# Performance work log

Hardware: AMD Instinct MI355X
Metric: run time of the kernel (lower is better)

Reference implementation:

```python
import jax, jax.numpy as jnp
import numpy as np

N_NODES = 20000
D = 256            # input_dim (forced by 32x16 reshape: 2*D == 512)
N_EDGES = 320000


def _init(key, shape, scale=0.02):
    return scale * jax.random.normal(key, shape, jnp.float32)


def setup_inputs() -> dict:
    key = jax.random.key(0)
    ks = jax.random.split(key, 20)
    x = jax.random.normal(ks[0], (N_NODES, D), jnp.float32)
    edge = jax.random.randint(ks[1], (N_EDGES, 2), 0, N_NODES, dtype=jnp.int64)
    params = dict(
        W_gcn=_init(ks[2], (D, 2 * D)), b_gcn=jnp.zeros((2 * D,), jnp.float32),
        conv1_w=_init(ks[3], (1, 1, 3, 3)), conv1_b=jnp.zeros((1,), jnp.float32),
        conv2_w=_init(ks[4], (1, 1, 3, 3)), conv2_b=jnp.zeros((1,), jnp.float32),
        Wc1=_init(ks[5], (2 * D, 2 * D)), bc1=jnp.zeros((2 * D,), jnp.float32),
        Wc2=_init(ks[6], (2 * D, 2 * D)), bc2=jnp.zeros((2 * D,), jnp.float32),
        Wc3=_init(ks[7], (2 * D, 2 * D)), bc3=jnp.zeros((2 * D,), jnp.float32),
        Wp1=_init(ks[8], (4 * D, 2 * D)), bp1=jnp.zeros((2 * D,), jnp.float32),
        Wp2=_init(ks[9], (2 * D, D)), bp2=jnp.zeros((D,), jnp.float32),
        Wp3=_init(ks[10], (D, D // 2)), bp3=jnp.zeros((D // 2,), jnp.float32),
        Wp4=_init(ks[11], (D // 2, 2)), bp4=jnp.zeros((2,), jnp.float32),
    )
    return dict(x=x, edge=edge, **params)


def _gcn_conv(x, edge, W, b):
    # PyG GCNConv: add self-loops, symmetric deg^-1/2 normalization, scatter-add at dst
    src, dst = edge[:, 0], edge[:, 1]
    loops = jnp.arange(N_NODES, dtype=edge.dtype)
    src = jnp.concatenate([src, loops])
    dst = jnp.concatenate([dst, loops])
    xw = x @ W                                              # [N, 2D]
    deg = jax.ops.segment_sum(jnp.ones_like(dst, jnp.float32), dst, N_NODES)
    dinv = jnp.where(deg > 0, jax.lax.rsqrt(jnp.maximum(deg, 1e-12)), 0.0)
    norm = dinv[src] * dinv[dst]                            # [E+N]
    agg = jax.ops.segment_sum(norm[:, None] * xw[src], dst, N_NODES)
    return agg + b


def reference(x, edge, W_gcn, b_gcn, conv1_w, conv1_b, conv2_w, conv2_b,
              Wc1, bc1, Wc2, bc2, Wc3, bc3,
              Wp1, bp1, Wp2, bp2, Wp3, bp3, Wp4, bp4):
    # First stage: GCNConv + ReLU, then sum readout over nodes -> [1, 2D]
    h = jax.nn.relu(_gcn_conv(x, edge, W_gcn, b_gcn))
    h = jnp.sum(h, axis=0, keepdims=True)                   # [1, 512]

    img = h.reshape(1, 1, 32, 16)
    dn = ('NCHW', 'OIHW', 'NCHW')
    c = jax.nn.relu(jax.lax.conv_general_dilated(img, conv1_w, (1, 1), 'SAME', dimension_numbers=dn) + conv1_b.reshape(1, -1, 1, 1))
    c = jax.nn.relu(jax.lax.conv_general_dilated(c, conv2_w, (1, 1), 'SAME', dimension_numbers=dn) + conv2_b.reshape(1, -1, 1, 1))
    high_conf = jax.nn.softmax(c.reshape(1, -1), axis=1)    # [1, 512]

    # Second stage, branch B: 3-layer MLP with softmax
    f = jax.nn.relu(h @ Wc1 + bc1)
    f = jax.nn.relu(f @ Wc2 + bc2)
    front = jax.nn.softmax(f @ Wc3 + bc3, axis=1)           # [1, 512]

    complete = jnp.concatenate([high_conf, front], axis=1)  # [1, 1024]

    # Predictor MLP: 1024 -> 512 -> 256 -> 128 -> 2, sigmoid
    p = jax.nn.relu(complete @ Wp1 + bp1)
    p = jax.nn.relu(p @ Wp2 + bp2)
    p = jax.nn.relu(p @ Wp3 + bp3)
    pre = jax.nn.sigmoid(p @ Wp4 + bp4)                     # [1, 2]
    return pre
```

## Files before the change

### kernel.cpp

```cpp
#include <hip/hip_runtime.h>

#define N_NODES 20000
#define N_EDGES 320000
#define DD      256
#define D2      512
#define BCAP    64

typedef short short8 __attribute__((ext_vector_type(8)));
typedef float f32x4  __attribute__((ext_vector_type(4)));
typedef float f32x2  __attribute__((ext_vector_type(2)));

__device__ __forceinline__ unsigned f2b(float f) {
    unsigned u = __float_as_uint(f);
    u = u + 0x7fffu + ((u >> 16) & 1u);
    return u >> 16;
}

__device__ __forceinline__ unsigned decode_cnt(unsigned c) {
    return (c >= 0xAAAAAAAAu) ? c - 0xAAAAAAAAu : c;
}

__device__ __forceinline__ void packW(const float* __restrict__ src, unsigned* __restrict__ dst,
                                      int i, int logn) {
    int N = 1 << logn;
    int c = i & (N - 1);
    int kp = i >> logn;
    const float* r0 = src + ((size_t)kp << (logn + 1)) + c;
    float4 a = *(const float4*)r0;
    float4 b = *(const float4*)(r0 + N);
    uint4 o;
    o.x = f2b(a.x) | (f2b(b.x) << 16);
    o.y = f2b(a.y) | (f2b(b.y) << 16);
    o.z = f2b(a.z) | (f2b(b.z) << 16);
    o.w = f2b(a.w) | (f2b(b.w) << 16);
    *(uint4*)(dst + i) = o;
}

__global__ void k1_prep(const int* __restrict__ edge, unsigned* __restrict__ cnt,
                        int* __restrict__ csr, const float* __restrict__ x,
                        const float* __restrict__ Wg, unsigned short* __restrict__ WT,
                        unsigned* __restrict__ xf8, int* __restrict__ zbase,
                        const float* __restrict__ Wc1, const float* __restrict__ Wc2,
                        const float* __restrict__ Wc3, const float* __restrict__ Wp1,
                        const float* __restrict__ Wp2, const float* __restrict__ Wp3,
                        unsigned* __restrict__ Wc1p, unsigned* __restrict__ Wc2p,
                        unsigned* __restrict__ Wc3p, unsigned* __restrict__ Wp1p,
                        unsigned* __restrict__ Wp2p, unsigned* __restrict__ Wp3p) {
    int blk = blockIdx.x, tid = threadIdx.x;
    if (blk < 1250) {
        int e = blk * 256 + tid;
        if (e < N_EDGES) {
            int s = edge[2 * e], d = edge[2 * e + 1];
            unsigned pos = atomicAdd(&cnt[d], 1u);
            unsigned rel = decode_cnt(pos);
            if (rel < BCAP) csr[d * BCAP + rel] = s;
        }
    } else if (blk < 1282) {
        int i = (blk - 1250) * 256 + tid;
        #pragma unroll
        for (int r = 0; r < 16; r++) {
            int idx = i + r * 8192;
            int k = idx >> 9, n = idx & 511;
            WT[n * 256 + k] = (unsigned short)f2b(Wg[idx]);
        }
    } else if (blk < 6282) {
        int i = (blk - 1282) * 256 + tid;
        float4 v = ((const float4*)x)[i];
        unsigned o = 0;
        o = __builtin_amdgcn_cvt_pk_fp8_f32(v.x, v.y, o, false);
        o = __builtin_amdgcn_cvt_pk_fp8_f32(v.z, v.w, o, true);
        xf8[i] = o;
    } else if (blk < 6285) {
        int i = (blk - 6282) * 256 + tid;
        if (i < 640) zbase[i] = 0;
    } else if (blk < 6413) { packW(Wc1, Wc1p, ((blk - 6285) * 256 + tid) * 4, 9); }
    else if (blk < 6541) { packW(Wc2, Wc2p, ((blk - 6413) * 256 + tid) * 4, 9); }
    else if (blk < 6669) { packW(Wc3, Wc3p, ((blk - 6541) * 256 + tid) * 4, 9); }
    else if (blk < 6925) { packW(Wp1, Wp1p, ((blk - 6669) * 256 + tid) * 4, 9); }
    else if (blk < 6989) { packW(Wp2, Wp2p, ((blk - 6925) * 256 + tid) * 4, 8); }
    else                 { packW(Wp3, Wp3p, ((blk - 6989) * 256 + tid) * 4, 7); }
}

__device__ __forceinline__ float dinv_of(const unsigned* cnt, int n) {
    return rsqrtf((float)(decode_cnt(cnt[n]) + 1u));
}
__device__ __forceinline__ void acc16p(f32x2* a, float w, uint4 u) {
    f32x2 wv = {w, w};
    unsigned uu[4] = {u.x, u.y, u.z, u.w};
    #pragma unroll
    for (int q = 0; q < 4; q++) {
        a[q * 2 + 0] += wv * __builtin_amdgcn_cvt_pk_f32_fp8(uu[q], false);
        a[q * 2 + 1] += wv * __builtin_amdgcn_cvt_pk_f32_fp8(uu[q], true);
    }
}

__global__ void k4_agg(const unsigned* __restrict__ cnt, const int* __restrict__ csr,
                       const unsigned char* __restrict__ xf8,
                       unsigned short* __restrict__ aggX) {
    int wid = threadIdx.x >> 6, lane = threadIdx.x & 63;
    int g = lane >> 4, l16 = lane & 15;
    int n = blockIdx.x * 4 + wid;
    f32x2 a[8];
    #pragma unroll
    for (int j = 0; j < 8; j++) a[j] = (f32x2){0.f, 0.f};
    if (n < N_NODES) {
        int deg = (int)decode_cnt(cnt[n]);
        if (deg > BCAP) deg = BCAP;
        const int* bkt = csr + n * BCAP;
        int e = 0;
        for (; e + 8 <= deg; e += 8) {
            int s0 = bkt[e + g], s1 = bkt[e + 4 + g];
            uint4 u0 = *(const uint4*)(xf8 + (size_t)s0 * DD + l16 * 16);
            uint4 u1 = *(const uint4*)(xf8 + (size_t)s1 * DD + l16 * 16);
            float w0 = dinv_of(cnt, s0), w1 = dinv_of(cnt, s1);
            acc16p(a, w0, u0); acc16p(a, w1, u1);
        }
        for (; e < deg; e += 4) {
            int idx = e + g;
            int cidx = idx < deg ? idx : deg - 1;
            int s = bkt[cidx];
            uint4 u = *(const uint4*)(xf8 + (size_t)s * DD + l16 * 16);
            float w = idx < deg ? dinv_of(cnt, s) : 0.f;
            acc16p(a, w, u);
        }
        #pragma unroll
        for (int j = 0; j < 8; j++) {
            a[j].x += __shfl_xor(a[j].x, 16, 64);
            a[j].x += __shfl_xor(a[j].x, 32, 64);
            a[j].y += __shfl_xor(a[j].y, 16, 64);
            a[j].y += __shfl_xor(a[j].y, 32, 64);
        }
        float dn = dinv_of(cnt, n), dn2 = dn * dn;
        f32x2 dv = {dn, dn}, dv2 = {dn2, dn2};
        uint4 u = *(const uint4*)(xf8 + (size_t)n * DD + l16 * 16);
        unsigned uu[4] = {u.x, u.y, u.z, u.w};
        #pragma unroll
        for (int q = 0; q < 4; q++) {
            a[q * 2 + 0] = dv * a[q * 2 + 0] + dv2 * __builtin_amdgcn_cvt_pk_f32_fp8(uu[q], false);
            a[q * 2 + 1] = dv * a[q * 2 + 1] + dv2 * __builtin_amdgcn_cvt_pk_f32_fp8(uu[q], true);
        }
    }
    if (g == 0) {
        unsigned o[8];
        #pragma unroll
        for (int j = 0; j < 8; j++) o[j] = f2b(a[j].x) | (f2b(a[j].y) << 16);
        uint4* dst = (uint4*)(aggX + (size_t)n * DD + l16 * 16);
        dst[0] = make_uint4(o[0], o[1], o[2], o[3]);
        dst[1] = make_uint4(o[4], o[5], o[6], o[7]);
    }
}

#define TN 128
#define BPAD 268
__global__ void __launch_bounds__(256, 2)
k5_gemm(const unsigned short* __restrict__ aggX, const unsigned short* __restrict__ WT,
        const float* __restrict__ bg, float* __restrict__ h) {
    __shared__ unsigned short bsh[TN * BPAD];
    __shared__ float hblk[TN];
    int tid = threadIdx.x;
    int rowblk = blockIdx.x;
    int ct = blockIdx.y;
    #pragma unroll
    for (int i = 0; i < 16; i++) {
        int c = tid + i * 256;
        int r = c >> 5;
        int kc = (c & 31) << 3;
        *(short8*)(&bsh[r * BPAD + kc]) = *(const short8*)(WT + (size_t)(ct * TN + r) * DD + kc);
    }
    if (tid < TN) hblk[tid] = 0.f;
    __syncthreads();

    int w = tid >> 6, lane = tid & 63;
    int quad = lane >> 4, l15 = lane & 15;
    int row0 = rowblk * 128 + w * 32 + l15;
    f32x4 acc[2][8];
    #pragma unroll
    for (int s = 0; s < 2; s++)
        #pragma unroll
        for (int nt = 0; nt < 8; nt++) acc[s][nt] = (f32x4){0.f, 0.f, 0.f, 0.f};
    #pragma unroll
    for (int kt = 0; kt < 8; kt++) {
        short8 a0 = *(const short8*)(aggX + (size_t)row0 * DD + kt * 32 + quad * 8);
        short8 a1 = *(const short8*)(aggX + (size_t)(row0 + 16) * DD + kt * 32 + quad * 8);
        #pragma unroll
        for (int nt = 0; nt < 8; nt++) {
            short8 b = *(const short8*)(&bsh[(nt * 16 + l15) * BPAD + kt * 32 + quad * 8]);
            acc[0][nt] = __builtin_amdgcn_mfma_f32_16x16x32_bf16(a0, b, acc[0][nt], 0, 0, 0);
            acc[1][nt] = __builtin_amdgcn_mfma_f32_16x16x32_bf16(a1, b, acc[1][nt], 0, 0, 0);
        }
    }
    #pragma unroll
    for (int s = 0; s < 2; s++) {
        int rowbase = rowblk * 128 + w * 32 + s * 16 + quad * 4;
        #pragma unroll
        for (int nt = 0; nt < 8; nt++) {
            int cl = nt * 16 + l15;
            float bias = bg[ct * TN + cl];
            float sum = 0.f;
            #pragma unroll
            for (int r = 0; r < 4; r++) {
                if (rowbase + r < N_NODES) {
                    float v = acc[s][nt][r] + bias;
                    sum += v > 0.f ? v : 0.f;
                }
            }
            sum += __shfl_xor(sum, 16, 64);
            sum += __shfl_xor(sum, 32, 64);
            if (quad == 0) atomicAdd(&hblk[cl], sum);
        }
    }
    __syncthreads();
    if (tid < TN) atomicAdd(&h[ct * TN + tid], hblk[tid]);
}

#define TB 16u
__device__ __forceinline__ void gbar(unsigned* bar, int idx) {
    __syncthreads();
    if (threadIdx.x == 0) {
        __threadfence();
        __hip_atomic_fetch_add(&bar[idx * 16], 1u, __ATOMIC_RELEASE, __HIP_MEMORY_SCOPE_AGENT);
        while (__hip_atomic_load(&bar[idx * 16], __ATOMIC_ACQUIRE, __HIP_MEMORY_SCOPE_AGENT) < TB)
            __builtin_amdgcn_s_sleep(2);
    }
    __syncthreads();
}

__device__ __forceinline__ float conv3(const float* im, const float* wgt, int idx) {
    int y = idx >> 4, x = idx & 15;
    float s = 0.f;
    #pragma unroll
    for (int dy = -1; dy <= 1; dy++)
        #pragma unroll
        for (int dx = -1; dx <= 1; dx++) {
            int yy = y + dy, xx = x + dx;
            if (yy >= 0 && yy < 32 && xx >= 0 && xx < 16)
                s += wgt[(dy + 1) * 3 + (dx + 1)] * im[yy * 16 + xx];
        }
    return s;
}

__device__ __forceinline__ void mv32(const float* vin, const unsigned* __restrict__ Wp,
                                     int Kh, int N, int cb, float* part, float* outv) {
    int t = threadIdx.x;
    int c = cb + (t & 31), sl = t >> 5;
    int kpn = Kh >> 3;
    const unsigned* wp = Wp + (size_t)(sl * kpn) * N + c;
    float acc = 0.f;
    #pragma unroll 8
    for (int j = 0; j < kpn; j++) {
        unsigned u = wp[(size_t)j * N];
        int k = (sl * kpn + j) * 2;
        acc += vin[k] * __uint_as_float(u << 16) + vin[k + 1] * __uint_as_float(u & 0xffff0000u);
    }
    part[t] = acc;
    __syncthreads();
    if (t < 32) {
        float s = part[t];
        #pragma unroll
        for (int q = 1; q < 8; q++) s += part[t + q * 32];
        outv[cb + t] = s;
    }
}

__global__ void __launch_bounds__(256)
kt_tail(const float* __restrict__ h,
        const float* __restrict__ c1w, const float* __restrict__ c1b,
        const float* __restrict__ c2w, const float* __restrict__ c2b,
        const float* __restrict__ bc1, const float* __restrict__ bc2, const float* __restrict__ bc3,
        const unsigned* __restrict__ Wc1p, const unsigned* __restrict__ Wc2p,
        const unsigned* __restrict__ Wc3p, const unsigned* __restrict__ Wp1p,
        const unsigned* __restrict__ Wp2p, const unsigned* __restrict__ Wp3p,
        const float* __restrict__ bp1, const float* __restrict__ bp2, const float* __restrict__ bp3,
        const float* __restrict__ Wp4, const float* __restrict__ bp4,
        float* __restrict__ f1raw, float* __restrict__ f2raw, float* __restrict__ l3raw,
        float* __restrict__ p1raw, float* __restrict__ p2raw,
        float* __restrict__ out, unsigned* __restrict__ bar) {
    __shared__ float himg[512], vin[512], part[256], compL[1024], red[256];
    int b = blockIdx.x, t = threadIdx.x;
    himg[t] = h[t]; himg[t + 256] = h[t + 256];
    __syncthreads();

    mv32(himg, Wc1p, 256, 512, b * 32, part, f1raw);
    gbar(bar, 0);

    vin[t] = fmaxf(f1raw[t] + bc1[t], 0.f);
    vin[t + 256] = fmaxf(f1raw[t + 256] + bc1[t + 256], 0.f);
    __syncthreads();
    mv32(vin, Wc2p, 256, 512, b * 32, part, f2raw);
    gbar(bar, 1);

    vin[t] = fmaxf(f2raw[t] + bc2[t], 0.f);
    vin[t + 256] = fmaxf(f2raw[t + 256] + bc2[t + 256], 0.f);
    __syncthreads();
    mv32(vin, Wc3p, 256, 512, b * 32, part, l3raw);
    gbar(bar, 2);

    {
        float cb1 = c1b[0], cb2 = c2b[0];
        vin[t] = fmaxf(conv3(himg, c1w, t) + cb1, 0.f);
        vin[t + 256] = fmaxf(conv3(himg, c1w, t + 256) + cb1, 0.f);
        __syncthreads();
        float v0 = fmaxf(conv3(vin, c2w, t) + cb2, 0.f);
        float v1 = fmaxf(conv3(vin, c2w, t + 256) + cb2, 0.f);
        red[t] = fmaxf(v0, v1); __syncthreads();
        for (int off = 128; off > 0; off >>= 1) { if (t < off) red[t] = fmaxf(red[t], red[t + off]); __syncthreads(); }
        float m = red[0]; __syncthreads();
        float e0 = expf(v0 - m), e1 = expf(v1 - m);
        red[t] = e0 + e1; __syncthreads();
        for (int off = 128; off > 0; off >>= 1) { if (t < off) red[t] += red[t + off]; __syncthreads(); }
        float inv = 1.f / red[0];
        compL[t] = e0 * inv; compL[t + 256] = e1 * inv;
        __syncthreads();
        float z0 = l3raw[t] + bc3[t], z1 = l3raw[t + 256] + bc3[t + 256];
        red[t] = fmaxf(z0, z1); __syncthreads();
        for (int off = 128; off > 0; off >>= 1) { if (t < off) red[t] = fmaxf(red[t], red[t + off]); __syncthreads(); }
        float m2 = red[0]; __syncthreads();
        float e2 = expf(z0 - m2), e3 = expf(z1 - m2);
        red[t] = e2 + e3; __syncthreads();
        for (int off = 128; off > 0; off >>= 1) { if (t < off) red[t] += red[t + off]; __syncthreads(); }
        float inv2 = 1.f / red[0];
        compL[512 + t] = e2 * inv2; compL[768 + t] = e3 * inv2;
    }
    __syncthreads();

    mv32(compL, Wp1p, 512, 512, b * 32, part, p1raw);
    gbar(bar, 3);

    vin[t] = fmaxf(p1raw[t] + bp1[t], 0.f);
    vin[t + 256] = fmaxf(p1raw[t + 256] + bp1[t + 256], 0.f);
    __syncthreads();
    {
        int c = b * 16 + (t & 15), sl = t >> 4;
        const unsigned* wp = Wp2p + (size_t)(sl * 16) * 256 + c;
        float acc = 0.f;
        #pragma unroll 8
        for (int j = 0; j < 16; j++) {
            unsigned u = wp[(size_t)j * 256];
            int k = (sl * 16 + j) * 2;
            acc += vin[k] * __uint_as_float(u << 16) + vin[k + 1] * __uint_as_float(u & 0xffff0000u);
        }
        part[t] = acc;
        __syncthreads();
        if (t < 16) {
            float s = part[t];
            #pragma unroll
            for (int q = 1; q < 16; q++) s += part[t + q * 16];
            p2raw[b * 16 + t] = s;
        }
    }
    gbar(bar, 4);

    if (b == 0) {
        vin[t] = fmaxf(p2raw[t] + bp2[t], 0.f);
        __syncthreads();
        if (t < 128) {
            float acc = 0.f;
            #pragma unroll 8
            for (int kp = 0; kp < 128; kp++) {
                unsigned u = Wp3p[kp * 128 + t];
                acc += vin[2 * kp] * __uint_as_float(u << 16)
                     + vin[2 * kp + 1] * __uint_as_float(u & 0xffff0000u);
            }
            red[t] = fmaxf(acc + bp3[t], 0.f);
        }
        __syncthreads();
        if (t < 2) {
            float s = bp4[t];
            #pragma unroll 8
            for (int k = 0; k < 128; k++) s += red[k] * Wp4[k * 2 + t];
            out[t] = 1.f / (1.f + expf(-s));
        }
    }
}

extern "C" void kernel_launch(void* const* d_in, const int* in_sizes, int n_in,
                              void* d_out, int out_size, void* d_ws, size_t ws_size,
                              hipStream_t stream) {
    const float* x    = (const float*)d_in[0];
    const int*   edge = (const int*)d_in[1];
    const float* Wg   = (const float*)d_in[2];
    const float* bg   = (const float*)d_in[3];
    const float* c1w  = (const float*)d_in[4];
    const float* c1b  = (const float*)d_in[5];
    const float* c2w  = (const float*)d_in[6];
    const float* c2b  = (const float*)d_in[7];
    const float* Wc1  = (const float*)d_in[8];
    const float* bc1  = (const float*)d_in[9];
    const float* Wc2  = (const float*)d_in[10];
    const float* bc2  = (const float*)d_in[11];
    const float* Wc3  = (const float*)d_in[12];
    const float* bc3  = (const float*)d_in[13];
    const float* Wp1  = (const float*)d_in[14];
    const float* bp1  = (const float*)d_in[15];
    const float* Wp2  = (const float*)d_in[16];
    const float* bp2  = (const float*)d_in[17];
    const float* Wp3  = (const float*)d_in[18];
    const float* bp3  = (const float*)d_in[19];
    const float* Wp4  = (const float*)d_in[20];
    const float* bp4  = (const float*)d_in[21];
    float* out = (float*)d_out;

    char* ws = (char*)d_ws;
    unsigned* cnt   = (unsigned*)(ws + 0);
    float* h        = (float*)(ws + 80000);
    unsigned* bar   = (unsigned*)(ws + 82048);
    float* f1raw    = (float*)(ws + 82560);
    float* f2raw    = (float*)(ws + 84608);
    float* l3raw    = (float*)(ws + 86656);
    float* p1raw    = (float*)(ws + 88704);
    float* p2raw    = (float*)(ws + 90752);
    int*   csr      = (int*)(ws + 91904);
    unsigned short* WT   = (unsigned short*)(ws + 5211904);
    unsigned char*  xf8  = (unsigned char*)(ws + 5474048);
    unsigned short* aggX = (unsigned short*)(ws + 10594048);
    unsigned* Wc1p  = (unsigned*)(ws + 20883200);
    unsigned* Wc2p  = (unsigned*)(ws + 21407488);
    unsigned* Wc3p  = (unsigned*)(ws + 21931776);
    unsigned* Wp1p  = (unsigned*)(ws + 22456064);
    unsigned* Wp2p  = (unsigned*)(ws + 23504640);
    unsigned* Wp3p  = (unsigned*)(ws + 23766784);
    (void)ws_size; (void)in_sizes; (void)n_in; (void)out_size;

    k1_prep<<<7005, 256, 0, stream>>>(edge, cnt, csr, x, Wg, WT, (unsigned*)xf8, (int*)h,
                                      Wc1, Wc2, Wc3, Wp1, Wp2, Wp3,
                                      Wc1p, Wc2p, Wc3p, Wp1p, Wp2p, Wp3p);
    k4_agg<<<5008, 256, 0, stream>>>(cnt, csr, xf8, aggX);
    k5_gemm<<<dim3(157, 4), 256, 0, stream>>>(aggX, WT, bg, h);
    kt_tail<<<16, 256, 0, stream>>>(h, c1w, c1b, c2w, c2b, bc1, bc2, bc3,
                                    Wc1p, Wc2p, Wc3p, Wp1p, Wp2p, Wp3p,
                                    bp1, bp2, bp3, Wp4, bp4,
                                    f1raw, f2raw, l3raw, p1raw, p2raw, out, bar);
}
```

Baseline: 197.0 us.

## Fuse GEMM and MLP tail into one kernel with grid barrier; unroll aggregation by 16

Merges the GEMM-readout kernel and the tail MLP kernel into one launch. Every GEMM block bumps a completion counter, and the first 16 blocks spin on it until all 628 GEMM blocks finish, then run the tail using reused shared memory. This removes one kernel launch and its inter-kernel gap. It relies on the first 16 blocks staying resident while the others finish, which is a forward-progress assumption and a deadlock risk. The edge aggregation loop also gets an extra 16-wide unrolled stage, giving more memory loads in flight per wave.

```diff
diff --git a/kernel.cpp b/kernel.cpp
--- a/kernel.cpp
+++ b/kernel.cpp
@@ -108,6 +108,16 @@
         if (deg > BCAP) deg = BCAP;
         const int* bkt = csr + n * BCAP;
         int e = 0;
+        for (; e + 16 <= deg; e += 16) {
+            int s0 = bkt[e + g], s1 = bkt[e + 4 + g], s2 = bkt[e + 8 + g], s3 = bkt[e + 12 + g];
+            uint4 u0 = *(const uint4*)(xf8 + (size_t)s0 * DD + l16 * 16);
+            uint4 u1 = *(const uint4*)(xf8 + (size_t)s1 * DD + l16 * 16);
+            uint4 u2 = *(const uint4*)(xf8 + (size_t)s2 * DD + l16 * 16);
+            uint4 u3 = *(const uint4*)(xf8 + (size_t)s3 * DD + l16 * 16);
+            float w0 = dinv_of(cnt, s0), w1 = dinv_of(cnt, s1);
+            float w2 = dinv_of(cnt, s2), w3 = dinv_of(cnt, s3);
+            acc16p(a, w0, u0); acc16p(a, w1, u1); acc16p(a, w2, u2); acc16p(a, w3, u3);
+        }
         for (; e + 8 <= deg; e += 8) {
             int s0 = bkt[e + g], s1 = bkt[e + 4 + g];
             uint4 u0 = *(const uint4*)(xf8 + (size_t)s0 * DD + l16 * 16);
@@ -152,14 +162,79 @@
 
 #define TN 128
 #define BPAD 268
+#define TB 16u
+#define GEMM_NB 628u
+
+__device__ __forceinline__ void gbar(unsigned* bar, int idx) {
+    __syncthreads();
+    if (threadIdx.x == 0) {
+        __threadfence();
+        __hip_atomic_fetch_add(&bar[idx * 16], 1u, __ATOMIC_RELEASE, __HIP_MEMORY_SCOPE_AGENT);
+        while (__hip_atomic_load(&bar[idx * 16], __ATOMIC_ACQUIRE, __HIP_MEMORY_SCOPE_AGENT) < TB)
+            __builtin_amdgcn_s_sleep(2);
+    }
+    __syncthreads();
+}
+
+__device__ __forceinline__ float conv3(const float* im, const float* wgt, int idx) {
+    int y = idx >> 4, x = idx & 15;
+    float s = 0.f;
+    #pragma unroll
+    for (int dy = -1; dy <= 1; dy++)
+        #pragma unroll
+        for (int dx = -1; dx <= 1; dx++) {
+            int yy = y + dy, xx = x + dx;
+            if (yy >= 0 && yy < 32 && xx >= 0 && xx < 16)
+                s += wgt[(dy + 1) * 3 + (dx + 1)] * im[yy * 16 + xx];
+        }
+    return s;
+}
+
+__device__ __forceinline__ void mv32(const float* vin, const unsigned* __restrict__ Wp,
+                                     int Kh, int N, int cb, float* part, float* outv) {
+    int t = threadIdx.x;
+    int c = cb + (t & 31), sl = t >> 5;
+    int kpn = Kh >> 3;
+    const unsigned* wp = Wp + (size_t)(sl * kpn) * N + c;
+    float acc = 0.f;
+    #pragma unroll 8
+    for (int j = 0; j < kpn; j++) {
+        unsigned u = wp[(size_t)j * N];
+        int k = (sl * kpn + j) * 2;
+        acc += vin[k] * __uint_as_float(u << 16) + vin[k + 1] * __uint_as_float(u & 0xffff0000u);
+    }
+    part[t] = acc;
+    __syncthreads();
+    if (t < 32) {
+        float s = part[t];
+        #pragma unroll
+        for (int q = 1; q < 8; q++) s += part[t + q * 32];
+        outv[cb + t] = s;
+    }
+}
+
 __global__ void __launch_bounds__(256, 2)
-k5_gemm(const unsigned short* __restrict__ aggX, const unsigned short* __restrict__ WT,
-        const float* __restrict__ bg, float* __restrict__ h) {
-    __shared__ unsigned short bsh[TN * BPAD];
-    __shared__ float hblk[TN];
+k5t(const unsigned short* __restrict__ aggX, const unsigned short* __restrict__ WT,
+    const float* __restrict__ bg, float* __restrict__ h,
+    const float* __restrict__ c1w, const float* __restrict__ c1b,
+    const float* __restrict__ c2w, const float* __restrict__ c2b,
+    const float* __restrict__ bc1, const float* __restrict__ bc2, const float* __restrict__ bc3,
+    const unsigned* __restrict__ Wc1p, const unsigned* __restrict__ Wc2p,
+    const unsigned* __restrict__ Wc3p, const unsigned* __restrict__ Wp1p,
+    const unsigned* __restrict__ Wp2p, const unsigned* __restrict__ Wp3p,
+    const float* __restrict__ bp1, const float* __restrict__ bp2, const float* __restrict__ bp3,
+    const float* __restrict__ Wp4, const float* __restrict__ bp4,
+    float* __restrict__ f1raw, float* __restrict__ f2raw, float* __restrict__ l3raw,
+    float* __restrict__ p1raw, float* __restrict__ p2raw,
+    float* __restrict__ out, unsigned* __restrict__ bar) {
+    __shared__ char smem[TN * BPAD * 2 + TN * 4];
+    unsigned short* bsh = (unsigned short*)smem;
+    float* hblk = (float*)(smem + TN * BPAD * 2);
     int tid = threadIdx.x;
-    int rowblk = blockIdx.x;
-    int ct = blockIdx.y;
+    int blk = blockIdx.x;
+    int rowblk = blk % 157;
+    int ct = blk / 157;
+
     #pragma unroll
     for (int i = 0; i < 16; i++) {
         int c = tid + i * 256;
@@ -211,72 +286,25 @@
     }
     __syncthreads();
     if (tid < TN) atomicAdd(&h[ct * TN + tid], hblk[tid]);
-}
-
-#define TB 16u
-__device__ __forceinline__ void gbar(unsigned* bar, int idx) {
-    __syncthreads();
-    if (threadIdx.x == 0) {
+
+    __syncthreads();
+    if (tid == 0) {
         __threadfence();
-        __hip_atomic_fetch_add(&bar[idx * 16], 1u, __ATOMIC_RELEASE, __HIP_MEMORY_SCOPE_AGENT);
-        while (__hip_atomic_load(&bar[idx * 16], __ATOMIC_ACQUIRE, __HIP_MEMORY_SCOPE_AGENT) < TB)
+        __hip_atomic_fetch_add(&bar[5 * 16], 1u, __ATOMIC_RELEASE, __HIP_MEMORY_SCOPE_AGENT);
+    }
+    if (blk >= 16) return;
+    if (tid == 0) {
+        while (__hip_atomic_load(&bar[5 * 16], __ATOMIC_ACQUIRE, __HIP_MEMORY_SCOPE_AGENT) < GEMM_NB)
             __builtin_amdgcn_s_sleep(2);
     }
     __syncthreads();
-}
-
-__device__ __forceinline__ float conv3(const float* im, const float* wgt, int idx) {
-    int y = idx >> 4, x = idx & 15;
-    float s = 0.f;
-    #pragma unroll
-    for (int dy = -1; dy <= 1; dy++)
-        #pragma unroll
-        for (int dx = -1; dx <= 1; dx++) {
-            int yy = y + dy, xx = x + dx;
-            if (yy >= 0 && yy < 32 && xx >= 0 && xx < 16)
-                s += wgt[(dy + 1) * 3 + (dx + 1)] * im[yy * 16 + xx];
-        }
-    return s;
-}
-
-__device__ __forceinline__ void mv32(const float* vin, const unsigned* __restrict__ Wp,
-                                     int Kh, int N, int cb, float* part, float* outv) {
-    int t = threadIdx.x;
-    int c = cb + (t & 31), sl = t >> 5;
-    int kpn = Kh >> 3;
-    const unsigned* wp = Wp + (size_t)(sl * kpn) * N + c;
-    float acc = 0.f;
-    #pragma unroll 8
-    for (int j = 0; j < kpn; j++) {
-        unsigned u = wp[(size_t)j * N];
-        int k = (sl * kpn + j) * 2;
-        acc += vin[k] * __uint_as_float(u << 16) + vin[k + 1] * __uint_as_float(u & 0xffff0000u);
-    }
-    part[t] = acc;
-    __syncthreads();
-    if (t < 32) {
-        float s = part[t];
-        #pragma unroll
-        for (int q = 1; q < 8; q++) s += part[t + q * 32];
-        outv[cb + t] = s;
-    }
-}
-
-__global__ void __launch_bounds__(256)
-kt_tail(const float* __restrict__ h,
-        const float* __restrict__ c1w, const float* __restrict__ c1b,
-        const float* __restrict__ c2w, const float* __restrict__ c2b,
-        const float* __restrict__ bc1, const float* __restrict__ bc2, const float* __restrict__ bc3,
-        const unsigned* __restrict__ Wc1p, const unsigned* __restrict__ Wc2p,
-        const unsigned* __restrict__ Wc3p, const unsigned* __restrict__ Wp1p,
-        const unsigned* __restrict__ Wp2p, const unsigned* __restrict__ Wp3p,
-        const float* __restrict__ bp1, const float* __restrict__ bp2, const float* __restrict__ bp3,
-        const float* __restrict__ Wp4, const float* __restrict__ bp4,
-        float* __restrict__ f1raw, float* __restrict__ f2raw, float* __restrict__ l3raw,
-        float* __restrict__ p1raw, float* __restrict__ p2raw,
-        float* __restrict__ out, unsigned* __restrict__ bar) {
-    __shared__ float himg[512], vin[512], part[256], compL[1024], red[256];
-    int b = blockIdx.x, t = threadIdx.x;
+
+    float* himg  = (float*)smem;
+    float* vin   = (float*)(smem + 2048);
+    float* part  = (float*)(smem + 4096);
+    float* compL = (float*)(smem + 5120);
+    float* red   = (float*)(smem + 9216);
+    int b = blk, t = tid;
     himg[t] = h[t]; himg[t + 256] = h[t + 256];
     __syncthreads();
 
@@ -332,14 +360,14 @@
     {
         int c = b * 16 + (t & 15), sl = t >> 4;
         const unsigned* wp = Wp2p + (size_t)(sl * 16) * 256 + c;
-        float acc = 0.f;
+        float acc2 = 0.f;
         #pragma unroll 8
         for (int j = 0; j < 16; j++) {
             unsigned u = wp[(size_t)j * 256];
             int k = (sl * 16 + j) * 2;
-            acc += vin[k] * __uint_as_float(u << 16) + vin[k + 1] * __uint_as_float(u & 0xffff0000u);
-        }
-        part[t] = acc;
+            acc2 += vin[k] * __uint_as_float(u << 16) + vin[k + 1] * __uint_as_float(u & 0xffff0000u);
+        }
+        part[t] = acc2;
         __syncthreads();
         if (t < 16) {
             float s = part[t];
@@ -354,14 +382,14 @@
         vin[t] = fmaxf(p2raw[t] + bp2[t], 0.f);
         __syncthreads();
         if (t < 128) {
-            float acc = 0.f;
+            float acc3 = 0.f;
             #pragma unroll 8
             for (int kp = 0; kp < 128; kp++) {
                 unsigned u = Wp3p[kp * 128 + t];
-                acc += vin[2 * kp] * __uint_as_float(u << 16)
-                     + vin[2 * kp + 1] * __uint_as_float(u & 0xffff0000u);
+                acc3 += vin[2 * kp] * __uint_as_float(u << 16)
+                      + vin[2 * kp + 1] * __uint_as_float(u & 0xffff0000u);
             }
-            red[t] = fmaxf(acc + bp3[t], 0.f);
+            red[t] = fmaxf(acc3 + bp3[t], 0.f);
         }
         __syncthreads();
         if (t < 2) {
@@ -425,9 +453,9 @@
                                       Wc1, Wc2, Wc3, Wp1, Wp2, Wp3,
                                       Wc1p, Wc2p, Wc3p, Wp1p, Wp2p, Wp3p);
     k4_agg<<<5008, 256, 0, stream>>>(cnt, csr, xf8, aggX);
-    k5_gemm<<<dim3(157, 4), 256, 0, stream>>>(aggX, WT, bg, h);
-    kt_tail<<<16, 256, 0, stream>>>(h, c1w, c1b, c2w, c2b, bc1, bc2, bc3,
-                                    Wc1p, Wc2p, Wc3p, Wp1p, Wp2p, Wp3p,
-                                    bp1, bp2, bp3, Wp4, bp4,
-                                    f1raw, f2raw, l3raw, p1raw, p2raw, out, bar);
-}
+    k5t<<<628, 256, 0, stream>>>(aggX, WT, bg, h,
+                                 c1w, c1b, c2w, c2b, bc1, bc2, bc3,
+                                 Wc1p, Wc2p, Wc3p, Wp1p, Wp2p, Wp3p,
+                                 bp1, bp2, bp3, Wp4, bp4,
+                                 f1raw, f2raw, l3raw, p1raw, p2raw, out, bar);
+}
```

New measurement: 233.1 us. 18.3% more time.

## Split prep kernel into streaming and bucketing kernels; preload neighbor indices via shuffles

Applied to the files above, without the earlier changes.

The combined prep kernel is split in two. One kernel does the streaming conversions (x to fp8, weight packing, zeroing), and a separate kernel does the atomic edge bucketing, launched afterward. In the aggregation kernel, each wave loads up to 64 neighbor indices and their degree weights in a single coalesced load, then broadcasts them with wave shuffles instead of reloading per round. This removes repeated bucket and count loads from the gather loop, at the cost of one extra kernel launch.

```diff
diff --git a/kernel.cpp b/kernel.cpp
--- a/kernel.cpp
+++ b/kernel.cpp
@@ -36,49 +36,53 @@
     *(uint4*)(dst + i) = o;
 }
 
-__global__ void k1_prep(const int* __restrict__ edge, unsigned* __restrict__ cnt,
-                        int* __restrict__ csr, const float* __restrict__ x,
-                        const float* __restrict__ Wg, unsigned short* __restrict__ WT,
-                        unsigned* __restrict__ xf8, int* __restrict__ zbase,
-                        const float* __restrict__ Wc1, const float* __restrict__ Wc2,
-                        const float* __restrict__ Wc3, const float* __restrict__ Wp1,
-                        const float* __restrict__ Wp2, const float* __restrict__ Wp3,
-                        unsigned* __restrict__ Wc1p, unsigned* __restrict__ Wc2p,
-                        unsigned* __restrict__ Wc3p, unsigned* __restrict__ Wp1p,
-                        unsigned* __restrict__ Wp2p, unsigned* __restrict__ Wp3p) {
+__global__ void k1b_stream(const float* __restrict__ x, unsigned* __restrict__ xf8,
+                           const float* __restrict__ Wg, unsigned short* __restrict__ WT,
+                           int* __restrict__ zbase,
+                           const float* __restrict__ Wc1, const float* __restrict__ Wc2,
+                           const float* __restrict__ Wc3, const float* __restrict__ Wp1,
+                           const float* __restrict__ Wp2, const float* __restrict__ Wp3,
+                           unsigned* __restrict__ Wc1p, unsigned* __restrict__ Wc2p,
+                           unsigned* __restrict__ Wc3p, unsigned* __restrict__ Wp1p,
+                           unsigned* __restrict__ Wp2p, unsigned* __restrict__ Wp3p) {
     int blk = blockIdx.x, tid = threadIdx.x;
-    if (blk < 1250) {
-        int e = blk * 256 + tid;
-        if (e < N_EDGES) {
-            int s = edge[2 * e], d = edge[2 * e + 1];
-            unsigned pos = atomicAdd(&cnt[d], 1u);
-            unsigned rel = decode_cnt(pos);
-            if (rel < BCAP) csr[d * BCAP + rel] = s;
-        }
-    } else if (blk < 1282) {
-        int i = (blk - 1250) * 256 + tid;
-        #pragma unroll
-        for (int r = 0; r < 16; r++) {
-            int idx = i + r * 8192;
-            int k = idx >> 9, n = idx & 511;
-            WT[n * 256 + k] = (unsigned short)f2b(Wg[idx]);
-        }
-    } else if (blk < 6282) {
-        int i = (blk - 1282) * 256 + tid;
+    if (blk < 5000) {
+        int i = blk * 256 + tid;
         float4 v = ((const float4*)x)[i];
         unsigned o = 0;
         o = __builtin_amdgcn_cvt_pk_fp8_f32(v.x, v.y, o, false);
         o = __builtin_amdgcn_cvt_pk_fp8_f32(v.z, v.w, o, true);
         xf8[i] = o;
-    } else if (blk < 6285) {
-        int i = (blk - 6282) * 256 + tid;
+    } else if (blk < 5032) {
+        int i = (blk - 5000) * 256 + tid;
+        #pragma unroll
+        for (int r = 0; r < 16; r++) {
+            int idx = i + r * 8192;
+            int k = idx >> 9, n = idx & 511;
+            WT[n * 256 + k] = (unsigned short)f2b(Wg[idx]);
+        }
+    }
+    else if (blk < 5160) { packW(Wc1, Wc1p, ((blk - 5032) * 256 + tid) * 4, 9); }
+    else if (blk < 5288) { packW(Wc2, Wc2p, ((blk - 5160) * 256 + tid) * 4, 9); }
+    else if (blk < 5416) { packW(Wc3, Wc3p, ((blk - 5288) * 256 + tid) * 4, 9); }
+    else if (blk < 5672) { packW(Wp1, Wp1p, ((blk - 5416) * 256 + tid) * 4, 9); }
+    else if (blk < 5736) { packW(Wp2, Wp2p, ((blk - 5672) * 256 + tid) * 4, 8); }
+    else if (blk < 5752) { packW(Wp3, Wp3p, ((blk - 5736) * 256 + tid) * 4, 7); }
+    else {
+        int i = (blk - 5752) * 256 + tid;
         if (i < 640) zbase[i] = 0;
-    } else if (blk < 6413) { packW(Wc1, Wc1p, ((blk - 6285) * 256 + tid) * 4, 9); }
-    else if (blk < 6541) { packW(Wc2, Wc2p, ((blk - 6413) * 256 + tid) * 4, 9); }
-    else if (blk < 6669) { packW(Wc3, Wc3p, ((blk - 6541) * 256 + tid) * 4, 9); }
-    else if (blk < 6925) { packW(Wp1, Wp1p, ((blk - 6669) * 256 + tid) * 4, 9); }
-    else if (blk < 6989) { packW(Wp2, Wp2p, ((blk - 6925) * 256 + tid) * 4, 8); }
-    else                 { packW(Wp3, Wp3p, ((blk - 6989) * 256 + tid) * 4, 7); }
+    }
+}
+
+__global__ void k1a_bucket(const int* __restrict__ edge, unsigned* __restrict__ cnt,
+                           int* __restrict__ csr) {
+    int e = blockIdx.x * 256 + threadIdx.x;
+    if (e < N_EDGES) {
+        int s = edge[2 * e], d = edge[2 * e + 1];
+        unsigned pos = atomicAdd(&cnt[d], 1u);
+        unsigned rel = decode_cnt(pos);
+        if (rel < BCAP) csr[d * BCAP + rel] = s;
+    }
 }
 
 __device__ __forceinline__ float dinv_of(const unsigned* cnt, int n) {
@@ -97,7 +101,8 @@
 __global__ void k4_agg(const unsigned* __restrict__ cnt, const int* __restrict__ csr,
                        const unsigned char* __restrict__ xf8,
                        unsigned short* __restrict__ aggX) {
-    int wid = threadIdx.x >> 6, lane = threadIdx.x & 63;
+    int tid = threadIdx.x;
+    int wid = tid >> 6, lane = tid & 63;
     int g = lane >> 4, l16 = lane & 15;
     int n = blockIdx.x * 4 + wid;
     f32x2 a[8];
@@ -107,21 +112,23 @@
         int deg = (int)decode_cnt(cnt[n]);
         if (deg > BCAP) deg = BCAP;
         const int* bkt = csr + n * BCAP;
-        int e = 0;
-        for (; e + 8 <= deg; e += 8) {
-            int s0 = bkt[e + g], s1 = bkt[e + 4 + g];
-            uint4 u0 = *(const uint4*)(xf8 + (size_t)s0 * DD + l16 * 16);
-            uint4 u1 = *(const uint4*)(xf8 + (size_t)s1 * DD + l16 * 16);
-            float w0 = dinv_of(cnt, s0), w1 = dinv_of(cnt, s1);
-            acc16p(a, w0, u0); acc16p(a, w1, u1);
-        }
-        for (; e < deg; e += 4) {
-            int idx = e + g;
-            int cidx = idx < deg ? idx : deg - 1;
-            int s = bkt[cidx];
-            uint4 u = *(const uint4*)(xf8 + (size_t)s * DD + l16 * 16);
-            float w = idx < deg ? dinv_of(cnt, s) : 0.f;
-            acc16p(a, w, u);
+        if (deg > 0) {
+            int li = lane < deg ? lane : deg - 1;
+            int sidx = bkt[li];
+            float sw = dinv_of(cnt, sidx);
+            int rounds = (deg + 7) >> 3;
+            for (int r = 0; r < rounds; r++) {
+                int i0 = r * 8 + g, i1 = r * 8 + 4 + g;
+                int c0 = i0 < deg ? i0 : deg - 1;
+                int c1 = i1 < deg ? i1 : deg - 1;
+                int s0 = __shfl(sidx, c0, 64);
+                int s1 = __shfl(sidx, c1, 64);
+                float w0 = i0 < deg ? __shfl(sw, c0, 64) : 0.f;
+                float w1 = i1 < deg ? __shfl(sw, c1, 64) : 0.f;
+                uint4 u0 = *(const uint4*)(xf8 + (size_t)s0 * DD + l16 * 16);
+                uint4 u1 = *(const uint4*)(xf8 + (size_t)s1 * DD + l16 * 16);
+                acc16p(a, w0, u0); acc16p(a, w1, u1);
+            }
         }
         #pragma unroll
         for (int j = 0; j < 8; j++) {
@@ -421,9 +428,10 @@
     unsigned* Wp3p  = (unsigned*)(ws + 23766784);
     (void)ws_size; (void)in_sizes; (void)n_in; (void)out_size;
 
-    k1_prep<<<7005, 256, 0, stream>>>(edge, cnt, csr, x, Wg, WT, (unsigned*)xf8, (int*)h,
-                                      Wc1, Wc2, Wc3, Wp1, Wp2, Wp3,
-                                      Wc1p, Wc2p, Wc3p, Wp1p, Wp2p, Wp3p);
+    k1b_stream<<<5755, 256, 0, stream>>>(x, (unsigned*)xf8, Wg, WT, (int*)h,
+                                         Wc1, Wc2, Wc3, Wp1, Wp2, Wp3,
+                                         Wc1p, Wc2p, Wc3p, Wp1p, Wp2p, Wp3p);
+    k1a_bucket<<<1250, 256, 0, stream>>>(edge, cnt, csr);
     k4_agg<<<5008, 256, 0, stream>>>(cnt, csr, xf8, aggX);
     k5_gemm<<<dim3(157, 4), 256, 0, stream>>>(aggX, WT, bg, h);
     kt_tail<<<16, 256, 0, stream>>>(h, c1w, c1b, c2w, c2b, bc1, bc2, bc3,
```

Result: slower. 201.4 us (+2.3%).
